# Kernel tuning notes

Hardware: AMD Instinct MI355X
Metric: run time of the kernel (lower is better)

The kernel has to match this reference:

```python
import jax, jax.numpy as jnp
import numpy as np

SIZES = [1024, 4096, 4096, 4096, 1024]  # layer widths
BATCH = 8192


def setup_inputs() -> dict:
    key = jax.random.key(0)
    keys = jax.random.split(key, 1 + 6 * 4)
    inp = {"x": jax.random.normal(keys[0], (BATCH, SIZES[0]), dtype=jnp.float32)}
    k = 1
    for j, (din, dout) in enumerate(zip(SIZES[:-1], SIZES[1:])):
        scale = 1.0 / np.sqrt(din)
        inp[f"mw{j}"] = jax.random.normal(keys[k], (dout, din), dtype=jnp.float32) * scale; k += 1
        inp[f"sw{j}"] = jax.random.normal(keys[k], (dout, din), dtype=jnp.float32) * scale; k += 1
        inp[f"zw{j}"] = jax.random.normal(keys[k], (dout, din), dtype=jnp.float32); k += 1
        inp[f"mb{j}"] = jax.random.normal(keys[k], (dout,), dtype=jnp.float32) * scale; k += 1
        inp[f"sb{j}"] = jax.random.normal(keys[k], (dout,), dtype=jnp.float32) * scale; k += 1
        inp[f"zb{j}"] = jax.random.normal(keys[k], (dout,), dtype=jnp.float32); k += 1
    return inp


def reference(x,
              mw0, sw0, zw0, mb0, sb0, zb0,
              mw1, sw1, zw1, mb1, sb1, zb1,
              mw2, sw2, zw2, mb2, sb2, zb2,
              mw3, sw3, zw3, mb3, sb3, zb3):
    layers = [
        (mw0, sw0, zw0, mb0, sb0, zb0),
        (mw1, sw1, zw1, mb1, sb1, zb1),
        (mw2, sw2, zw2, mb2, sb2, zb2),
        (mw3, sw3, zw3, mb3, sb3, zb3),
    ]
    n = len(layers)
    h = x
    for j, (mw, sw, zw, mb, sb, zb) in enumerate(layers):
        # rho(sigma) = log(1 + exp(sigma)) == softplus; reparameterized weight sample
        A = mw + jax.nn.softplus(sw) * zw          # [out, in]
        b = mb + jax.nn.softplus(sb) * zb          # [out]
        h = h @ A.T + b                             # [B, out]
        if j < n - 1:                               # activation between Linear layers
            h = jnp.tanh(h)
    return h
```

## Files before the change

kernel.cpp:

```cpp
#include <hip/hip_runtime.h>
#include <cstdint>
#include <cstddef>

typedef _Float16 f16;
typedef _Float16 f16x8 __attribute__((ext_vector_type(8)));
typedef float    fx4   __attribute__((ext_vector_type(4)));


__device__ __forceinline__ float softplus_f(float x) {
    return (x > 20.0f) ? x : log1pf(expf(x));
}

__global__ void prep_w_kernel(const float* __restrict__ mw, const float* __restrict__ sw,
                              const float* __restrict__ zw, f16* __restrict__ hi,
                              f16* __restrict__ lo, int n) {
    int i = (blockIdx.x * blockDim.x + threadIdx.x) * 4;
    if (i >= n) return;
    float4 m4 = *(const float4*)(mw + i);
    float4 s4 = *(const float4*)(sw + i);
    float4 z4 = *(const float4*)(zw + i);
    float a[4];
    a[0] = m4.x + softplus_f(s4.x) * z4.x;
    a[1] = m4.y + softplus_f(s4.y) * z4.y;
    a[2] = m4.z + softplus_f(s4.z) * z4.z;
    a[3] = m4.w + softplus_f(s4.w) * z4.w;
    f16 h4[4], l4[4];
#pragma unroll
    for (int j = 0; j < 4; ++j) {
        h4[j] = (f16)a[j];
        l4[j] = (f16)(a[j] - (float)h4[j]);
    }
    *(short4*)(hi + i) = *(short4*)h4;
    if (lo) *(short4*)(lo + i) = *(short4*)l4;
}

__global__ void prep_b_kernel(const float* __restrict__ mb, const float* __restrict__ sb,
                              const float* __restrict__ zb, float* __restrict__ b, int n) {
    int i = blockIdx.x * blockDim.x + threadIdx.x;
    if (i < n) b[i] = mb[i] + softplus_f(sb[i]) * zb[i];
}

__global__ void split_x_kernel(const float* __restrict__ x, f16* __restrict__ hi,
                               f16* __restrict__ lo, int n) {
    int i = (blockIdx.x * blockDim.x + threadIdx.x) * 4;
    if (i >= n) return;
    float4 v = *(const float4*)(x + i);
    float a[4] = {v.x, v.y, v.z, v.w};
    f16 h4[4], l4[4];
#pragma unroll
    for (int j = 0; j < 4; ++j) {
        h4[j] = (f16)a[j];
        l4[j] = (f16)(a[j] - (float)h4[j]);
    }
    *(short4*)(hi + i) = *(short4*)h4;
    *(short4*)(lo + i) = *(short4*)l4;
}

__device__ __forceinline__ void cp16(const f16* g, f16* l) {
    __builtin_amdgcn_global_load_lds((__attribute__((address_space(1))) void*)g,
                                     (__attribute__((address_space(3))) void*)l,
                                     16, 0, 0);
}


template <int SPLIT, int OUT>
__global__ __launch_bounds__(512, 2) void gemm256_kernel(
    const f16* __restrict__ Hhi, const f16* __restrict__ Hlo,
    const f16* __restrict__ Whi, const f16* __restrict__ Wlo,
    const float* __restrict__ bias,
    f16* __restrict__ Ohi, f16* __restrict__ Olo, float* __restrict__ Of,
    int M, int N, int K)
{
    __shared__ __align__(16) f16 lds[4][2][8192];

    const int tid  = threadIdx.x;
    const int lane = tid & 63;
    const int wave = tid >> 6;
    const int wm   = wave >> 2;
    const int wn   = wave & 3;
    const int col  = lane & 15;
    const int quad = lane >> 4;

    const int nwg = gridDim.x * gridDim.y;
    const int bid = blockIdx.y * gridDim.x + blockIdx.x;
    const int swz = (bid & 7) * (nwg >> 3) + (bid >> 3);
    const int bx  = swz % gridDim.x;
    const int by  = swz / gridDim.x;
    const int mBase = by * 256;
    const int nBase = bx * 256;

    const int    srow = tid >> 2;
    const int    kc   = (tid & 3) ^ ((tid >> 3) & 3);
    const size_t aoff0 = (size_t)(mBase + srow) * K + kc * 8;
    const size_t aoff1 = aoff0 + (size_t)128 * K;
    const size_t boff0 = (size_t)(nBase + srow) * K + kc * 8;
    const size_t boff1 = boff0 + (size_t)128 * K;

    const int NT = (SPLIT ? 3 : 1) * (K >> 5);

    auto stageA = [&](int j) {
        const f16* src; int k0;
        if constexpr (SPLIT) { int kb = j / 3, p = j - kb * 3; src = (p == 2) ? Hlo : Hhi; k0 = kb * 32; }
        else                 { src = Hhi; k0 = j * 32; }
        f16* d = &lds[j & 3][0][0];
        cp16(src + aoff0 + k0, d + tid * 8);
        cp16(src + aoff1 + k0, d + tid * 8 + 4096);
    };
    auto stageB = [&](int j) {
        const f16* src; int k0;
        if constexpr (SPLIT) { int kb = j / 3, p = j - kb * 3; src = (p == 1) ? Wlo : Whi; k0 = kb * 32; }
        else                 { src = Whi; k0 = j * 32; }
        f16* d = &lds[j & 3][1][0];
        cp16(src + boff0 + k0, d + tid * 8);
        cp16(src + boff1 + k0, d + tid * 8 + 4096);
    };

    stageA(0); stageB(0); stageA(1); stageB(1); stageA(2); stageB(2);

    float bias_v[4];
#pragma unroll
    for (int nf = 0; nf < 4; ++nf)
        bias_v[nf] = bias[nBase + wn * 64 + nf * 16 + col];

    fx4 acc[8][4];
#pragma unroll
    for (int i = 0; i < 8; ++i)
#pragma unroll
        for (int j = 0; j < 4; ++j)
            acc[i][j] = (fx4){0.f, 0.f, 0.f, 0.f};

    const int lane_off = col * 32 + ((quad ^ ((col >> 1) & 3)) << 3);
    const int aRow = wm * 128;
    const int bRow = wn * 64;

    for (int s = 0; s < NT; ++s) {
        if (s < NT - 2)       asm volatile("s_waitcnt vmcnt(8)" ::: "memory");
        else if (s == NT - 2) asm volatile("s_waitcnt vmcnt(4)" ::: "memory");
        else                  asm volatile("s_waitcnt vmcnt(0)" ::: "memory");
        __builtin_amdgcn_s_barrier();

        const f16* As = &lds[s & 3][0][0];
        const f16* Bs = &lds[s & 3][1][0];

        f16x8 bfr[4], afr[4];
#pragma unroll
        for (int nf = 0; nf < 4; ++nf)
            bfr[nf] = *(const f16x8*)&Bs[(bRow + nf * 16) * 32 + lane_off];
#pragma unroll
        for (int mf = 0; mf < 4; ++mf)
            afr[mf] = *(const f16x8*)&As[(aRow + mf * 16) * 32 + lane_off];
        if (s + 3 < NT) stageA(s + 3);

        __builtin_amdgcn_s_setprio(1);
#pragma unroll
        for (int mf = 0; mf < 4; ++mf)
#pragma unroll
            for (int nf = 0; nf < 4; ++nf)
                acc[mf][nf] = __builtin_amdgcn_mfma_f32_16x16x32_f16(afr[mf], bfr[nf], acc[mf][nf], 0, 0, 0);
        __builtin_amdgcn_s_setprio(0);

#pragma unroll
        for (int mf = 0; mf < 4; ++mf)
            afr[mf] = *(const f16x8*)&As[(aRow + 64 + mf * 16) * 32 + lane_off];
        if (s + 3 < NT) stageB(s + 3);

        __builtin_amdgcn_s_setprio(1);
#pragma unroll
        for (int mf = 0; mf < 4; ++mf)
#pragma unroll
            for (int nf = 0; nf < 4; ++nf)
                acc[4 + mf][nf] = __builtin_amdgcn_mfma_f32_16x16x32_f16(afr[mf], bfr[nf], acc[4 + mf][nf], 0, 0, 0);
        __builtin_amdgcn_s_setprio(0);
    }

#pragma unroll
    for (int mf = 0; mf < 8; ++mf)
#pragma unroll
        for (int nf = 0; nf < 4; ++nf) {
            const int n = nBase + wn * 64 + nf * 16 + col;
#pragma unroll
            for (int r = 0; r < 4; ++r) {
                const int m = mBase + wm * 128 + mf * 16 + quad * 4 + r;
                float v = acc[mf][nf][r] + bias_v[nf];
                size_t idx = (size_t)m * N + n;
                if constexpr (OUT == 2) {
                    Of[idx] = v;
                } else {
                    float t = tanhf(v);
                    f16 thi = (f16)t;
                    Ohi[idx] = thi;
                    if constexpr (OUT == 1) Olo[idx] = (f16)(t - (float)thi);
                }
            }
        }
}


template <int SPLIT, int OUT>
__global__ __launch_bounds__(256) void gemm_kernel(
    const f16* __restrict__ Hhi, const f16* __restrict__ Hlo,
    const f16* __restrict__ Whi, const f16* __restrict__ Wlo,
    const float* __restrict__ bias,
    f16* __restrict__ Ohi, f16* __restrict__ Olo, float* __restrict__ Of,
    int M, int N, int K)
{
    constexpr int LDSN = 128 * 32;
    __shared__ __align__(16) f16 Hs[(SPLIT ? 2 : 1) * LDSN];
    __shared__ __align__(16) f16 Ws[(SPLIT ? 2 : 1) * LDSN];

    const int tid  = threadIdx.x;
    const int lane = tid & 63;
    const int wave = tid >> 6;
    const int wm   = wave >> 1;
    const int wn   = wave & 1;
    const int col  = lane & 15;
    const int quad = lane >> 4;
    const int mBase = blockIdx.y * 128;
    const int nBase = blockIdx.x * 128;

    float bias_v[4];
#pragma unroll
    for (int nt = 0; nt < 4; ++nt)
        bias_v[nt] = bias[nBase + wn * 64 + nt * 16 + col];

    fx4 acc[4][4];
#pragma unroll
    for (int i = 0; i < 4; ++i)
#pragma unroll
        for (int j = 0; j < 4; ++j)
            acc[i][j] = (fx4){0.f, 0.f, 0.f, 0.f};

    const int c0 = wave * 128 + lane;

    for (int k0 = 0; k0 < K; k0 += 32) {
        __syncthreads();
#pragma unroll
        for (int i = 0; i < 2; ++i) {
            int c  = c0 + i * 64;
            int r  = c >> 2;
            int cc = c & 3;
            size_t gh = (size_t)(mBase + r) * K + k0 + cc * 8;
            size_t gw = (size_t)(nBase + r) * K + k0 + cc * 8;
            cp16(Hhi + gh, &Hs[c * 8]);
            cp16(Whi + gw, &Ws[c * 8]);
            if constexpr (SPLIT) {
                cp16(Hlo + gh, &Hs[LDSN + c * 8]);
                cp16(Wlo + gw, &Ws[LDSN + c * 8]);
            }
        }
        __syncthreads();

        f16x8 bh[4], bl[4];
#pragma unroll
        for (int nt = 0; nt < 4; ++nt) {
            int off = (wn * 64 + nt * 16 + col) * 32 + quad * 8;
            bh[nt] = *(const f16x8*)&Ws[off];
            if constexpr (SPLIT) bl[nt] = *(const f16x8*)&Ws[LDSN + off];
        }
#pragma unroll
        for (int mt = 0; mt < 4; ++mt) {
            int off = (wm * 64 + mt * 16 + col) * 32 + quad * 8;
            f16x8 ah = *(const f16x8*)&Hs[off];
            f16x8 al;
            if constexpr (SPLIT) al = *(const f16x8*)&Hs[LDSN + off];
#pragma unroll
            for (int nt = 0; nt < 4; ++nt) {
                acc[mt][nt] = __builtin_amdgcn_mfma_f32_16x16x32_f16(ah, bh[nt], acc[mt][nt], 0, 0, 0);
                if constexpr (SPLIT) {
                    acc[mt][nt] = __builtin_amdgcn_mfma_f32_16x16x32_f16(ah, bl[nt], acc[mt][nt], 0, 0, 0);
                    acc[mt][nt] = __builtin_amdgcn_mfma_f32_16x16x32_f16(al, bh[nt], acc[mt][nt], 0, 0, 0);
                }
            }
        }
    }

#pragma unroll
    for (int mt = 0; mt < 4; ++mt) {
#pragma unroll
        for (int nt = 0; nt < 4; ++nt) {
            int n = nBase + wn * 64 + nt * 16 + col;
#pragma unroll
            for (int r = 0; r < 4; ++r) {
                int m = mBase + wm * 64 + mt * 16 + quad * 4 + r;
                float v = acc[mt][nt][r] + bias_v[nt];
                size_t idx = (size_t)m * N + n;
                if constexpr (OUT == 2) {
                    Of[idx] = v;
                } else {
                    float t = tanhf(v);
                    f16 thi = (f16)t;
                    Ohi[idx] = thi;
                    if constexpr (OUT == 1) Olo[idx] = (f16)(t - (float)thi);
                }
            }
        }
    }
}


extern "C" void kernel_launch(void* const* d_in, const int* in_sizes, int n_in,
                              void* d_out, int out_size, void* d_ws, size_t ws_size,
                              hipStream_t stream) {
    const int BATCH = 8192;
    const int sizes[5] = {1024, 4096, 4096, 4096, 1024};

    char* ws = (char*)d_ws;
    f16*   x_hi  = (f16*)(ws + 0);
    f16*   x_lo  = (f16*)(ws + 16777216ULL);
    f16*   A0_hi = (f16*)(ws + 33554432ULL);
    f16*   A0_lo = (f16*)(ws + 41943040ULL);
    f16*   A_hi  = (f16*)(ws + 0);
    f16*   A_lo  = (f16*)(ws + 33554432ULL);
    f16*   H0_hi = (f16*)(ws + 67108864ULL);
    f16*   H0_lo = (f16*)(ws + 134217728ULL);
    f16*   H1_hi = (f16*)(ws + 201326592ULL);
    f16*   H2_hi = (f16*)(ws + 67108864ULL);
    float* bb    = (float*)(ws + 268435456ULL);

    const float* x = (const float*)d_in[0];
    const float* p[4][6];
    for (int j = 0; j < 4; ++j)
        for (int t = 0; t < 6; ++t)
            p[j][t] = (const float*)d_in[1 + j * 6 + t];

    {
        int n = BATCH * sizes[0];
        split_x_kernel<<<n / 4 / 256, 256, 0, stream>>>(x, x_hi, x_lo, n);
    }

    {
        int n = sizes[1] * sizes[0];
        prep_w_kernel<<<n / 4 / 256, 256, 0, stream>>>(p[0][0], p[0][1], p[0][2], A0_hi, A0_lo, n);
        prep_b_kernel<<<(sizes[1] + 255) / 256, 256, 0, stream>>>(p[0][3], p[0][4], p[0][5], bb, sizes[1]);
        dim3 grid(sizes[1] / 256, BATCH / 256);
        gemm256_kernel<1, 1><<<grid, 512, 0, stream>>>(
            x_hi, x_lo, A0_hi, A0_lo, bb, H0_hi, H0_lo, nullptr, BATCH, sizes[1], sizes[0]);
    }

    {
        int n = sizes[2] * sizes[1];
        prep_w_kernel<<<n / 4 / 256, 256, 0, stream>>>(p[1][0], p[1][1], p[1][2], A_hi, A_lo, n);
        prep_b_kernel<<<(sizes[2] + 255) / 256, 256, 0, stream>>>(p[1][3], p[1][4], p[1][5], bb, sizes[2]);
        dim3 grid(sizes[2] / 256, BATCH / 256);
        gemm256_kernel<1, 0><<<grid, 512, 0, stream>>>(
            H0_hi, H0_lo, A_hi, A_lo, bb, H1_hi, nullptr, nullptr, BATCH, sizes[2], sizes[1]);
    }

    {
        int n = sizes[3] * sizes[2];
        prep_w_kernel<<<n / 4 / 256, 256, 0, stream>>>(p[2][0], p[2][1], p[2][2], A_hi, nullptr, n);
        prep_b_kernel<<<(sizes[3] + 255) / 256, 256, 0, stream>>>(p[2][3], p[2][4], p[2][5], bb, sizes[3]);
        dim3 grid(sizes[3] / 256, BATCH / 256);
        gemm256_kernel<0, 0><<<grid, 512, 0, stream>>>(
            H1_hi, nullptr, A_hi, nullptr, bb, H2_hi, nullptr, nullptr, BATCH, sizes[3], sizes[2]);
    }

    {
        int n = sizes[4] * sizes[3];
        prep_w_kernel<<<n / 4 / 256, 256, 0, stream>>>(p[3][0], p[3][1], p[3][2], A_hi, nullptr, n);
        prep_b_kernel<<<(sizes[4] + 255) / 256, 256, 0, stream>>>(p[3][3], p[3][4], p[3][5], bb, sizes[4]);
        dim3 grid(sizes[4] / 128, BATCH / 128);
        gemm_kernel<0, 2><<<grid, 256, 0, stream>>>(
            H2_hi, nullptr, A_hi, nullptr, bb, nullptr, nullptr, (float*)d_out, BATCH, sizes[4], sizes[3]);
    }
}
```

Measured before the change: 1.734 ms.

## Add dedicated split-fp16 GEMM kernel that reuses hi fragments across three products

Adds a dedicated kernel for the split-precision (hi/lo) GEMM layers. Each K-block stages Hhi, Whi, Wlo and Hlo together into a double-buffered 64KB LDS region. Inside a block the Hhi fragments are reused for the hi*hi and hi*lo products and the Whi fragments for the lo*hi product, instead of three separate pipeline stages that each reload both operands. The new kernel uses one workgroup per CU with 8x4 fragments per wave, trading occupancy and register pressure for fewer LDS reads and barriers. The old kernel is reduced to the non-split path and gains a sched_barrier after its sync.

```diff
diff --git a/kernel.cpp b/kernel.cpp
--- a/kernel.cpp
+++ b/kernel.cpp
@@ -63,6 +63,149 @@
 }
 
 
+#define PHASE_SYNC(V)                                          \
+    asm volatile("s_waitcnt vmcnt(" V ")" ::: "memory");       \
+    __builtin_amdgcn_s_barrier();                              \
+    __builtin_amdgcn_sched_barrier(0);
+
+template <int OUT>
+__global__ __launch_bounds__(512, 1) void gemm256_split3_kernel(
+    const f16* __restrict__ Hhi, const f16* __restrict__ Hlo,
+    const f16* __restrict__ Whi, const f16* __restrict__ Wlo,
+    const float* __restrict__ bias,
+    f16* __restrict__ Ohi, f16* __restrict__ Olo,
+    int M, int N, int K)
+{
+    __shared__ __align__(16) f16 lds[2][4][8192];
+
+    const int tid  = threadIdx.x;
+    const int lane = tid & 63;
+    const int wave = tid >> 6;
+    const int wm   = wave >> 2;
+    const int wn   = wave & 3;
+    const int col  = lane & 15;
+    const int quad = lane >> 4;
+
+    const int nwg = gridDim.x * gridDim.y;
+    const int bid = blockIdx.y * gridDim.x + blockIdx.x;
+    const int swz = (bid & 7) * (nwg >> 3) + (bid >> 3);
+    const int bx  = swz % gridDim.x;
+    const int by  = swz / gridDim.x;
+    const int mBase = by * 256;
+    const int nBase = bx * 256;
+
+    const int    srow = tid >> 2;
+    const int    kc   = (tid & 3) ^ ((tid >> 3) & 3);
+    const size_t aoff0 = (size_t)(mBase + srow) * K + kc * 8;
+    const size_t aoff1 = aoff0 + (size_t)128 * K;
+    const size_t boff0 = (size_t)(nBase + srow) * K + kc * 8;
+    const size_t boff1 = boff0 + (size_t)128 * K;
+
+    const int NK = K >> 5;
+
+    auto stage = [&](int j) {
+        f16* d = &lds[j & 1][0][0];
+        const int k0 = j * 32;
+        cp16(Hhi + aoff0 + k0, d + tid * 8);
+        cp16(Hhi + aoff1 + k0, d + tid * 8 + 4096);
+        cp16(Whi + boff0 + k0, d + 8192  + tid * 8);
+        cp16(Whi + boff1 + k0, d + 8192  + tid * 8 + 4096);
+        cp16(Wlo + boff0 + k0, d + 16384 + tid * 8);
+        cp16(Wlo + boff1 + k0, d + 16384 + tid * 8 + 4096);
+        cp16(Hlo + aoff0 + k0, d + 24576 + tid * 8);
+        cp16(Hlo + aoff1 + k0, d + 24576 + tid * 8 + 4096);
+    };
+
+    float bias_v[4];
+#pragma unroll
+    for (int nf = 0; nf < 4; ++nf)
+        bias_v[nf] = bias[nBase + wn * 64 + nf * 16 + col];
+
+    stage(0);
+
+    fx4 acc[8][4];
+#pragma unroll
+    for (int i = 0; i < 8; ++i)
+#pragma unroll
+        for (int j = 0; j < 4; ++j)
+            acc[i][j] = (fx4){0.f, 0.f, 0.f, 0.f};
+
+    const int lane_off = col * 32 + ((quad ^ ((col >> 1) & 3)) << 3);
+    const int aRow = wm * 128;
+    const int bRow = wn * 64;
+
+    f16x8 ah[8], bh[4], bl[4], al[8];
+
+#define KB_BODY(V0, V1, V2, DO_STAGE, KB)                                          \
+    {                                                                              \
+        PHASE_SYNC(V0)                                                             \
+        if (DO_STAGE) stage((KB) + 1);                                             \
+        const f16* P = &lds[(KB) & 1][0][0];                                       \
+        _Pragma("unroll")                                                          \
+        for (int nf = 0; nf < 4; ++nf)                                             \
+            bh[nf] = *(const f16x8*)&P[8192 + (bRow + nf * 16) * 32 + lane_off];   \
+        _Pragma("unroll")                                                          \
+        for (int mf = 0; mf < 8; ++mf)                                             \
+            ah[mf] = *(const f16x8*)&P[(aRow + mf * 16) * 32 + lane_off];          \
+        __builtin_amdgcn_s_setprio(1);                                             \
+        _Pragma("unroll")                                                          \
+        for (int mf = 0; mf < 8; ++mf)                                             \
+            _Pragma("unroll")                                                      \
+            for (int nf = 0; nf < 4; ++nf)                                         \
+                acc[mf][nf] = __builtin_amdgcn_mfma_f32_16x16x32_f16(              \
+                    ah[mf], bh[nf], acc[mf][nf], 0, 0, 0);                         \
+        __builtin_amdgcn_s_setprio(0);                                             \
+        PHASE_SYNC(V1)                                                             \
+        _Pragma("unroll")                                                          \
+        for (int nf = 0; nf < 4; ++nf)                                             \
+            bl[nf] = *(const f16x8*)&P[16384 + (bRow + nf * 16) * 32 + lane_off];  \
+        __builtin_amdgcn_s_setprio(1);                                             \
+        _Pragma("unroll")                                                          \
+        for (int mf = 0; mf < 8; ++mf)                                             \
+            _Pragma("unroll")                                                      \
+            for (int nf = 0; nf < 4; ++nf)                                         \
+                acc[mf][nf] = __builtin_amdgcn_mfma_f32_16x16x32_f16(              \
+                    ah[mf], bl[nf], acc[mf][nf], 0, 0, 0);                         \
+        __builtin_amdgcn_s_setprio(0);                                             \
+        PHASE_SYNC(V2)                                                             \
+        _Pragma("unroll")                                                          \
+        for (int mf = 0; mf < 8; ++mf)                                             \
+            al[mf] = *(const f16x8*)&P[24576 + (aRow + mf * 16) * 32 + lane_off];  \
+        __builtin_amdgcn_s_setprio(1);                                             \
+        _Pragma("unroll")                                                          \
+        for (int mf = 0; mf < 8; ++mf)                                             \
+            _Pragma("unroll")                                                      \
+            for (int nf = 0; nf < 4; ++nf)                                         \
+                acc[mf][nf] = __builtin_amdgcn_mfma_f32_16x16x32_f16(              \
+                    al[mf], bh[nf], acc[mf][nf], 0, 0, 0);                         \
+        __builtin_amdgcn_s_setprio(0);                                             \
+    }
+
+    for (int kb = 0; kb + 1 < NK; ++kb)
+        KB_BODY("4", "10", "8", true, kb)
+    KB_BODY("4", "2", "0", false, NK - 1)
+
+#undef KB_BODY
+
+#pragma unroll
+    for (int mf = 0; mf < 8; ++mf)
+#pragma unroll
+        for (int nf = 0; nf < 4; ++nf) {
+            const int n = nBase + wn * 64 + nf * 16 + col;
+#pragma unroll
+            for (int r = 0; r < 4; ++r) {
+                const int m = mBase + wm * 128 + mf * 16 + quad * 4 + r;
+                float v = acc[mf][nf][r] + bias_v[nf];
+                size_t idx = (size_t)m * N + n;
+                float t = tanhf(v);
+                f16 thi = (f16)t;
+                Ohi[idx] = thi;
+                if constexpr (OUT == 1) Olo[idx] = (f16)(t - (float)thi);
+            }
+        }
+}
+
+
 template <int SPLIT, int OUT>
 __global__ __launch_bounds__(512, 2) void gemm256_kernel(
     const f16* __restrict__ Hhi, const f16* __restrict__ Hlo,
@@ -96,23 +239,17 @@
     const size_t boff0 = (size_t)(nBase + srow) * K + kc * 8;
     const size_t boff1 = boff0 + (size_t)128 * K;
 
-    const int NT = (SPLIT ? 3 : 1) * (K >> 5);
+    const int NT = K >> 5;
 
     auto stageA = [&](int j) {
-        const f16* src; int k0;
-        if constexpr (SPLIT) { int kb = j / 3, p = j - kb * 3; src = (p == 2) ? Hlo : Hhi; k0 = kb * 32; }
-        else                 { src = Hhi; k0 = j * 32; }
         f16* d = &lds[j & 3][0][0];
-        cp16(src + aoff0 + k0, d + tid * 8);
-        cp16(src + aoff1 + k0, d + tid * 8 + 4096);
+        cp16(Hhi + aoff0 + j * 32, d + tid * 8);
+        cp16(Hhi + aoff1 + j * 32, d + tid * 8 + 4096);
     };
     auto stageB = [&](int j) {
-        const f16* src; int k0;
-        if constexpr (SPLIT) { int kb = j / 3, p = j - kb * 3; src = (p == 1) ? Wlo : Whi; k0 = kb * 32; }
-        else                 { src = Whi; k0 = j * 32; }
         f16* d = &lds[j & 3][1][0];
-        cp16(src + boff0 + k0, d + tid * 8);
-        cp16(src + boff1 + k0, d + tid * 8 + 4096);
+        cp16(Whi + boff0 + j * 32, d + tid * 8);
+        cp16(Whi + boff1 + j * 32, d + tid * 8 + 4096);
     };
 
     stageA(0); stageB(0); stageA(1); stageB(1); stageA(2); stageB(2);
@@ -138,6 +275,7 @@
         else if (s == NT - 2) asm volatile("s_waitcnt vmcnt(4)" ::: "memory");
         else                  asm volatile("s_waitcnt vmcnt(0)" ::: "memory");
         __builtin_amdgcn_s_barrier();
+        __builtin_amdgcn_sched_barrier(0);
 
         const f16* As = &lds[s & 3][0][0];
         const f16* Bs = &lds[s & 3][1][0];
@@ -333,8 +471,8 @@
         prep_w_kernel<<<n / 4 / 256, 256, 0, stream>>>(p[0][0], p[0][1], p[0][2], A0_hi, A0_lo, n);
         prep_b_kernel<<<(sizes[1] + 255) / 256, 256, 0, stream>>>(p[0][3], p[0][4], p[0][5], bb, sizes[1]);
         dim3 grid(sizes[1] / 256, BATCH / 256);
-        gemm256_kernel<1, 1><<<grid, 512, 0, stream>>>(
-            x_hi, x_lo, A0_hi, A0_lo, bb, H0_hi, H0_lo, nullptr, BATCH, sizes[1], sizes[0]);
+        gemm256_split3_kernel<1><<<grid, 512, 0, stream>>>(
+            x_hi, x_lo, A0_hi, A0_lo, bb, H0_hi, H0_lo, BATCH, sizes[1], sizes[0]);
     }
 
     {
@@ -342,8 +480,8 @@
         prep_w_kernel<<<n / 4 / 256, 256, 0, stream>>>(p[1][0], p[1][1], p[1][2], A_hi, A_lo, n);
         prep_b_kernel<<<(sizes[2] + 255) / 256, 256, 0, stream>>>(p[1][3], p[1][4], p[1][5], bb, sizes[2]);
         dim3 grid(sizes[2] / 256, BATCH / 256);
-        gemm256_kernel<1, 0><<<grid, 512, 0, stream>>>(
-            H0_hi, H0_lo, A_hi, A_lo, bb, H1_hi, nullptr, nullptr, BATCH, sizes[2], sizes[1]);
+        gemm256_split3_kernel<0><<<grid, 512, 0, stream>>>(
+            H0_hi, H0_lo, A_hi, A_lo, bb, H1_hi, nullptr, BATCH, sizes[2], sizes[1]);
     }
 
     {
```

New measurement: 1.725 ms. No clear change (-0.5%).
